# Performance work log

Measured on AMD Instinct MI355X. Metric: run time of the kernel, lower is better.

The kernel has to match this reference:

```python
import jax, jax.numpy as jnp
import numpy as np

B, N, D = 8, 1024, 256
H = 8
DH = D // H
R = 4          # relation types 0..3; adj value 4 = no relation
FF = 1024
EPS = 1e-5


def _lin(k, fan_in, shape):
    return jax.random.normal(k, shape, jnp.float32) * (1.0 / np.sqrt(fan_in))


def setup_inputs() -> dict:
    key = jax.random.key(0)
    ks = jax.random.split(key, 16)
    src = jax.random.normal(ks[0], (B, N, D), jnp.float32)
    adj_matrix = jax.random.randint(ks[1], (B, N, N), 0, 5, dtype=jnp.int32)
    Wq = _lin(ks[2], D, (D, D)); bq = jnp.zeros((D,), jnp.float32)
    Wk = _lin(ks[3], D, (D, D)); bk = jnp.zeros((D,), jnp.float32)
    Wv = _lin(ks[4], D, (R, D, D)); bv = jnp.zeros((R, D), jnp.float32)
    Wo = _lin(ks[5], D, (D, D)); bo = jnp.zeros((D,), jnp.float32)
    W1 = _lin(ks[6], D, (D, FF)); b1 = jnp.zeros((FF,), jnp.float32)
    W2 = _lin(ks[7], FF, (FF, D)); b2 = jnp.zeros((D,), jnp.float32)
    g1 = jnp.ones((D,), jnp.float32); beta1 = jnp.zeros((D,), jnp.float32)
    g2 = jnp.ones((D,), jnp.float32); beta2 = jnp.zeros((D,), jnp.float32)
    return dict(src=src, adj_matrix=adj_matrix, Wq=Wq, bq=bq, Wk=Wk, bk=bk,
                Wv=Wv, bv=bv, Wo=Wo, bo=bo, W1=W1, b1=b1, W2=W2, b2=b2,
                g1=g1, beta1=beta1, g2=g2, beta2=beta2)


def _ln(x, g, b):
    m = x.mean(-1, keepdims=True)
    v = ((x - m) ** 2).mean(-1, keepdims=True)
    return (x - m) * jax.lax.rsqrt(v + EPS) * g + b


def reference(src, adj_matrix, Wq, bq, Wk, bk, Wv, bv, Wo, bo, W1, b1, W2, b2, g1, beta1, g2, beta2):
    Bb, Nn, Dm = src.shape
    h, dh = H, Dm // H
    q = (src @ Wq + bq).reshape(Bb, Nn, h, dh).transpose(0, 2, 1, 3)  # (B,H,N,dh)
    k = (src @ Wk + bk).reshape(Bb, Nn, h, dh).transpose(0, 2, 1, 3)
    scores = jnp.einsum('bhid,bhjd->bhij', q, k) / np.sqrt(dh)
    attn = jax.nn.softmax(scores, axis=-1)                             # (B,H,N,N)
    out = jnp.zeros_like(q)
    for r in range(Wv.shape[0]):  # small fixed relation loop, matches module
        v_r = (src @ Wv[r] + bv[r]).reshape(Bb, Nn, h, dh).transpose(0, 2, 1, 3)
        mask = (adj_matrix == r)[:, None]                              # (B,1,N,N)
        out = out + jnp.einsum('bhij,bhjd->bhid', attn * mask, v_r)
    attn_out = out.transpose(0, 2, 1, 3).reshape(Bb, Nn, Dm) @ Wo + bo
    x = _ln(src + attn_out, g1, beta1)
    ff = jax.nn.gelu(x @ W1 + b1, approximate=False) @ W2 + b2
    return _ln(x + ff, g2, beta2)
```

## Files before the change

kernel.cpp:

```cpp
#include <hip/hip_runtime.h>
#include <hip/hip_bf16.h>
#include <cmath>

constexpr int CB  = 8;
constexpr int CN  = 1024;
constexpr int CD  = 256;
constexpr int CH  = 8;
constexpr int CDH = 32;
constexpr int CR  = 4;
constexpr int CFF = 1024;
constexpr float CEPS = 1e-5f;
constexpr size_t SZH = (size_t)CB * CH * CN * CDH;

#define MODE_QK    0
#define MODE_OPROJ 1
#define MODE_FFN1  2
#define MODE_FFN2  3
#define MODE_VT    4

typedef float v4f __attribute__((ext_vector_type(4)));
typedef short v8s __attribute__((ext_vector_type(8)));

static __device__ __forceinline__ short f2bf(float f) {
    unsigned u = __builtin_bit_cast(unsigned, f);
    u += 0x7fff + ((u >> 16) & 1);
    return (short)(u >> 16);
}

static __device__ __forceinline__ void async_copy16(const void* g, void* l) {
    __builtin_amdgcn_global_load_lds(
        (const __attribute__((address_space(1))) void*)g,
        (__attribute__((address_space(3))) void*)l, 16, 0, 0);
}

template<int BM, int BN, int MODE>
__device__ __forceinline__ void gemm_body(
    const short* __restrict__ A, const short* __restrict__ Bw,
    const float* __restrict__ biasv, const float* __restrict__ add,
    void* __restrict__ dest, int M, int K, int Nw, int bx, int by, short* smem)
{
    constexpr int WTM = BM / 2, WTN = BN / 2;
    constexpr int TM = WTM / 16, TN = WTN / 16;
    short* As = smem;
    short* Bs = smem + 2 * BM * 32;

    const int t    = threadIdx.x;
    const int lane = t & 63;
    const int w    = t >> 6;
    const int quad = lane >> 4, l15 = lane & 15;
    const int wm = w >> 1, wn = w & 1;
    const int m0 = bx * BM, n0 = by * BN;

    const int srow = lane >> 2;
    const int scol = (lane & 3) * 8;

    v4f acc[TM][TN];
    #pragma unroll
    for (int i = 0; i < TM; ++i)
        #pragma unroll
        for (int j = 0; j < TN; ++j) acc[i][j] = (v4f){0.f, 0.f, 0.f, 0.f};

    const int NK = K >> 5;

    auto stage = [&](int buf, int kt) {
        #pragma unroll
        for (int u = 0; u < BM / 64; ++u) {
            const int e0 = (w * (BM / 64) + u) * 512;
            const int row = (e0 >> 5) + srow;
            async_copy16(A + (size_t)(m0 + row) * K + kt + scol,
                         &As[buf * BM * 32 + e0]);
        }
        #pragma unroll
        for (int u = 0; u < BN / 64; ++u) {
            const int e0 = (w * (BN / 64) + u) * 512;
            const int row = (e0 >> 5) + srow;
            async_copy16(Bw + (size_t)(n0 + row) * K + kt + scol,
                         &Bs[buf * BN * 32 + e0]);
        }
    };

    stage(0, 0);

    for (int it = 0; it < NK; ++it) {
        __syncthreads();
        if (it + 1 < NK) stage((it + 1) & 1, (it + 1) << 5);

        const int buf = it & 1;
        v8s af[TM], bfr[TN];
        #pragma unroll
        for (int i = 0; i < TM; ++i)
            af[i] = *(const v8s*)&As[buf * BM * 32 +
                                     (wm * WTM + i * 16 + l15) * 32 + quad * 8];
        #pragma unroll
        for (int j = 0; j < TN; ++j)
            bfr[j] = *(const v8s*)&Bs[buf * BN * 32 +
                                      (wn * WTN + j * 16 + l15) * 32 + quad * 8];
        #pragma unroll
        for (int i = 0; i < TM; ++i)
            #pragma unroll
            for (int j = 0; j < TN; ++j)
                acc[i][j] = __builtin_amdgcn_mfma_f32_16x16x32_bf16(
                    af[i], bfr[j], acc[i][j], 0, 0, 0);
    }

    #pragma unroll
    for (int i = 0; i < TM; ++i) {
        #pragma unroll
        for (int j = 0; j < TN; ++j) {
            const int mb = m0 + wm * WTM + i * 16 + quad * 4;
            const int n  = n0 + wn * WTN + j * 16 + l15;
            float vals[4];
            if (MODE == MODE_VT) {
                #pragma unroll
                for (int rr = 0; rr < 4; ++rr) vals[rr] = acc[i][j][rr] + biasv[mb + rr];
            } else {
                #pragma unroll
                for (int rr = 0; rr < 4; ++rr) vals[rr] = acc[i][j][rr] + biasv[n];
            }

            if (MODE == MODE_QK) {
                const int b = mb >> 10, ii0 = mb & 1023;
                const int plane = n >> 8, nn = n & 255;
                const int h = nn >> 5, d = nn & 31;
                #pragma unroll
                for (int rr = 0; rr < 4; ++rr)
                    ((short*)dest)[(size_t)plane * SZH +
                        (((size_t)(b * CH + h)) * CN + ii0 + rr) * CDH + d] =
                        f2bf(vals[rr]);
            } else if (MODE == MODE_VT) {
                const int b = n >> 10, ii = n & 1023;
                #pragma unroll
                for (int rr = 0; rr < 4; ++rr) {
                    const int m = mb + rr;
                    const int r2 = m >> 8, hd = m & 255;
                    const int h = hd >> 5, d = hd & 31;
                    ((short*)dest)[2 * SZH +
                        (((size_t)(r2 * 64 + b * CH + h)) * CDH + d) * CN + ii] =
                        f2bf(vals[rr]);
                }
            } else if (MODE == MODE_OPROJ || MODE == MODE_FFN2) {
                #pragma unroll
                for (int rr = 0; rr < 4; ++rr) {
                    const size_t idx = (size_t)(mb + rr) * Nw + n;
                    ((float*)dest)[idx] = vals[rr] + add[idx];
                }
            } else {
                #pragma unroll
                for (int rr = 0; rr < 4; ++rr) {
                    const size_t idx = (size_t)(mb + rr) * Nw + n;
                    const float xx = vals[rr];
                    const float E = exp2f(2.302217f * (xx + 0.044715f * xx * xx * xx));
                    ((short*)dest)[idx] = f2bf(xx * E / (E + 1.f));
                }
            }
        }
    }
}

template<int BM, int BN, int MODE>
__global__ __launch_bounds__(256)
void gemm_mfma(const short* __restrict__ A, const short* __restrict__ Bw,
               const float* __restrict__ biasv, const float* __restrict__ add,
               void* __restrict__ dest, int M, int K, int Nw)
{
    extern __shared__ short smem[];
    gemm_body<BM, BN, MODE>(A, Bw, biasv, add, dest, M, K, Nw,
                            blockIdx.x, blockIdx.y, smem);
}

__global__ __launch_bounds__(256)
void proj_kernel(const short* __restrict__ src_bf, const short* __restrict__ wqkvT,
                 const float* __restrict__ bpack, short* __restrict__ qkv)
{
    extern __shared__ short smem[];
    const int g = blockIdx.x;
    if (g < 512) {
        gemm_body<64, 128, MODE_QK>(src_bf, wqkvT, bpack, nullptr, qkv,
                                    8192, 256, 512, g >> 2, g & 3, smem);
    } else {
        const int h2 = g - 512;
        gemm_body<64, 128, MODE_VT>(wqkvT + 512 * 256, src_bf, bpack + 512, nullptr,
                                    qkv, 1024, 256, 8192, h2 & 15, h2 >> 4, smem);
    }
}

__global__ __launch_bounds__(256)
void prep(const int* __restrict__ adj, const float* __restrict__ src,
          const float* __restrict__ Wq, const float* __restrict__ Wk,
          const float* __restrict__ Wv, const float* __restrict__ Wo,
          const float* __restrict__ W1, const float* __restrict__ W2,
          const float* __restrict__ bq, const float* __restrict__ bk,
          const float* __restrict__ bv, const float* __restrict__ bo,
          const float* __restrict__ b1, const float* __restrict__ b2,
          unsigned char* __restrict__ adj8, short* __restrict__ src_bf,
          short* __restrict__ wqkvT, short* __restrict__ woT,
          short* __restrict__ w1T, short* __restrict__ w2T,
          float* __restrict__ bpack)
{
    const int bx = blockIdx.x, t = threadIdx.x;
    if (bx < 8192) {
        const int i = bx * 256 + t;
        const int4 vv = ((const int4*)adj)[i];
        uchar4 c;
        c.x = (unsigned char)vv.x; c.y = (unsigned char)vv.y;
        c.z = (unsigned char)vv.z; c.w = (unsigned char)vv.w;
        ((uchar4*)adj8)[i] = c;
    } else if (bx < 10240) {
        const int i = (bx - 8192) * 256 + t;
        const float4 v = ((const float4*)src)[i];
        short4 o;
        o.x = f2bf(v.x); o.y = f2bf(v.y); o.z = f2bf(v.z); o.w = f2bf(v.w);
        ((short4*)src_bf)[i] = o;
    } else if (bx < 11776) {
        const int idx = (bx - 10240) * 256 + t;
        const int n = idx >> 8, k = idx & 255;
        float v;
        if (n < 256)      v = Wq[k * 256 + n];
        else if (n < 512) v = Wk[k * 256 + (n - 256)];
        else { const int r = (n - 512) >> 8;
               v = Wv[((size_t)r * 256 + k) * 256 + ((n - 512) & 255)]; }
        wqkvT[idx] = f2bf(v);
    } else if (bx < 12032) {
        const int idx = (bx - 11776) * 256 + t;
        const int n = idx >> 8, k = idx & 255;
        woT[idx] = f2bf(Wo[k * 256 + n]);
    } else if (bx < 13056) {
        const int idx = (bx - 12032) * 256 + t;
        const int n = idx >> 8, k = idx & 255;
        w1T[idx] = f2bf(W1[k * 1024 + n]);
    } else if (bx < 14080) {
        const int idx = (bx - 13056) * 256 + t;
        const int n = idx >> 10, k = idx & 1023;
        w2T[idx] = f2bf(W2[k * 256 + n]);
    } else {
        const int idx = (bx - 14080) * 256 + t;
        float bvv;
        if (idx < 256)       bvv = bq[idx];
        else if (idx < 512)  bvv = bk[idx - 256];
        else if (idx < 1536) bvv = bv[idx - 512];
        else if (idx < 1792) bvv = bo[idx - 1536];
        else if (idx < 2816) bvv = b1[idx - 1792];
        else                 bvv = b2[idx - 2816];
        bpack[idx] = bvv;
    }
}

__global__ __launch_bounds__(256)
void attn_mfma(const short* __restrict__ qg, const short* __restrict__ kg,
               const short* __restrict__ vt, const unsigned char* __restrict__ adj8,
               short* __restrict__ outh)
{
    __shared__ __align__(16) short ks[64 * 32];
    __shared__ __align__(16) short vtile[4][32][72];
    __shared__ __align__(16) short ps[64][68];
    __shared__ __align__(16) unsigned char adjs[64][72];
    __shared__ int lut[64][4];

    const int t    = threadIdx.x;
    const int lane = t & 63;
    const int w    = t >> 6;
    const int quad = lane >> 4;
    const int l15  = lane & 15;
    const int i0   = blockIdx.x * 64;
    const int h    = blockIdx.y;
    const int b    = blockIdx.z;
    const int bhh  = b * CH + h;
    const size_t bh = (size_t)bhh;

    if (t < 64) {
        const int b0 = t & 7, b1 = t >> 3;
        #pragma unroll
        for (int r = 0; r < 4; ++r) {
            const int lo = (b0 == r) ? 0x0100 : 0x0c0c;
            const int hi = (b1 == r) ? 0x0302 : 0x0c0c;
            lut[t][r] = lo | (hi << 16);
        }
    }

    const v8s qfrag = *(const v8s*)&qg[(bh * CN + i0 + 16 * w + l15) * CDH + quad * 8];

    v4f oacc[2];
    oacc[0] = (v4f){0.f, 0.f, 0.f, 0.f};
    oacc[1] = (v4f){0.f, 0.f, 0.f, 0.f};
    float plsum[4] = {0.f, 0.f, 0.f, 0.f};

    const float cs = 0.25503480f;
    const int arow = 16 * w + l15;

    const int srow = lane >> 2;
    const int scol = (lane & 3) * 8;
    const int vd0  = lane >> 3;
    const int vc   = (lane & 7) * 8;
    const short* vplane = vt + (((size_t)(w * 64 + bhh)) * CDH) * CN;
    const int aro = t >> 2;
    const int aco = (t & 3) * 16;

    for (int jt = 0; jt < 16; ++jt) {
        const int j0 = jt * 64;
        __syncthreads();

        async_copy16(kg + (bh * CN + j0 + 16 * w + srow) * CDH + scol,
                     &ks[(16 * w + srow) * 32]);
        #pragma unroll
        for (int it = 0; it < 4; ++it) {
            const int d = vd0 + 8 * it;
            const v8s vv = *(const v8s*)&vplane[(size_t)d * CN + j0 + vc];
            *(v8s*)&vtile[w][d][vc] = vv;
        }
        const int4 av = *(const int4*)&adj8[((size_t)b * CN + i0 + aro) * CN + j0 + aco];
        *(int4*)&adjs[aro][aco] = av;
        __syncthreads();

        v4f sacc[4];
        #pragma unroll
        for (int jb = 0; jb < 4; ++jb) {
            const v8s kfrag = *(const v8s*)&ks[(16 * jb + l15) * 32 + quad * 8];
            sacc[jb] = __builtin_amdgcn_mfma_f32_16x16x32_bf16(
                qfrag, kfrag, (v4f){0.f, 0.f, 0.f, 0.f}, 0, 0, 0);
        }

        #pragma unroll
        for (int rr = 0; rr < 4; ++rr) {
            const int prow = 16 * w + quad * 4 + rr;
            float p[4];
            #pragma unroll
            for (int jb = 0; jb < 4; ++jb) p[jb] = exp2f(cs * sacc[jb][rr]);
            plsum[rr] += (p[0] + p[1]) + (p[2] + p[3]);
            #pragma unroll
            for (int jb = 0; jb < 4; ++jb)
                ps[prow][16 * jb + l15] = f2bf(p[jb]);
        }

        #pragma unroll
        for (int kb = 0; kb < 2; ++kb) {
            const int2 p0 = *(const int2*)&ps[arow][32 * kb + quad * 8];
            const int2 p1 = *(const int2*)&ps[arow][32 * kb + quad * 8 + 4];
            const int2 ab = *(const int2*)&adjs[arow][32 * kb + quad * 8];
            int pf[4][4];
            #pragma unroll
            for (int half = 0; half < 2; ++half) {
                const unsigned a = (unsigned)(half ? ab.y : ab.x);
                const int P0 = half ? p1.x : p0.x;
                const int P1 = half ? p1.y : p0.y;
                const int idxA = (a & 7) | ((a >> 5) & 0x38);
                const int idxB = ((a >> 16) & 7) | ((a >> 21) & 0x38);
                const int4 selA = *(const int4*)&lut[idxA][0];
                const int4 selB = *(const int4*)&lut[idxB][0];
                pf[0][half * 2 + 0] = __builtin_amdgcn_perm(P0, P0, selA.x);
                pf[1][half * 2 + 0] = __builtin_amdgcn_perm(P0, P0, selA.y);
                pf[2][half * 2 + 0] = __builtin_amdgcn_perm(P0, P0, selA.z);
                pf[3][half * 2 + 0] = __builtin_amdgcn_perm(P0, P0, selA.w);
                pf[0][half * 2 + 1] = __builtin_amdgcn_perm(P1, P1, selB.x);
                pf[1][half * 2 + 1] = __builtin_amdgcn_perm(P1, P1, selB.y);
                pf[2][half * 2 + 1] = __builtin_amdgcn_perm(P1, P1, selB.z);
                pf[3][half * 2 + 1] = __builtin_amdgcn_perm(P1, P1, selB.w);
            }
            #pragma unroll
            for (int r = 0; r < 4; ++r) {
                const v8s pfr = __builtin_bit_cast(v8s,
                    make_int4(pf[r][0], pf[r][1], pf[r][2], pf[r][3]));
                #pragma unroll
                for (int cb = 0; cb < 2; ++cb) {
                    const v8s vfrag = *(const v8s*)&vtile[r][16 * cb + l15][32 * kb + quad * 8];
                    oacc[cb] = __builtin_amdgcn_mfma_f32_16x16x32_bf16(
                        pfr, vfrag, oacc[cb], 0, 0, 0);
                }
            }
        }
    }

    #pragma unroll
    for (int rr = 0; rr < 4; ++rr) {
        float l = plsum[rr];
        #pragma unroll
        for (int off = 1; off < 16; off <<= 1) l += __shfl_xor(l, off);
        const float inv = 1.f / l;
        const int row = i0 + 16 * w + quad * 4 + rr;
        #pragma unroll
        for (int cb = 0; cb < 2; ++cb)
            outh[((size_t)b * CN + row) * CD + h * CDH + 16 * cb + l15] =
                f2bf(oacc[cb][rr] * inv);
    }
}

__global__ __launch_bounds__(256)
void ln_kernel(const float* __restrict__ in, const float* __restrict__ g,
               const float* __restrict__ be, float* __restrict__ out,
               short* __restrict__ outb)
{
    __shared__ float red[4];
    const int row = blockIdx.x;
    const int t = threadIdx.x;
    const float x = in[(size_t)row * CD + t];

    float s = x;
    #pragma unroll
    for (int off = 32; off > 0; off >>= 1) s += __shfl_xor(s, off);
    if ((t & 63) == 0) red[t >> 6] = s;
    __syncthreads();
    const float mean = (red[0] + red[1] + red[2] + red[3]) * (1.f / CD);
    __syncthreads();

    const float dx = x - mean;
    float s2 = dx * dx;
    #pragma unroll
    for (int off = 32; off > 0; off >>= 1) s2 += __shfl_xor(s2, off);
    if ((t & 63) == 0) red[t >> 6] = s2;
    __syncthreads();
    const float var = (red[0] + red[1] + red[2] + red[3]) * (1.f / CD);

    const float y = dx * rsqrtf(var + CEPS) * g[t] + be[t];
    out[(size_t)row * CD + t] = y;
    if (outb) outb[(size_t)row * CD + t] = f2bf(y);
}

extern "C" void kernel_launch(void* const* d_in, const int* in_sizes, int n_in,
                              void* d_out, int out_size, void* d_ws, size_t ws_size,
                              hipStream_t stream)
{
    const float* src = (const float*)d_in[0];
    const int*   adj = (const int*)d_in[1];
    const float* Wq  = (const float*)d_in[2];
    const float* bq  = (const float*)d_in[3];
    const float* Wk  = (const float*)d_in[4];
    const float* bk  = (const float*)d_in[5];
    const float* Wv  = (const float*)d_in[6];
    const float* bv  = (const float*)d_in[7];
    const float* Wo  = (const float*)d_in[8];
    const float* bo  = (const float*)d_in[9];
    const float* W1  = (const float*)d_in[10];
    const float* b1  = (const float*)d_in[11];
    const float* W2  = (const float*)d_in[12];
    const float* b2  = (const float*)d_in[13];
    const float* g1  = (const float*)d_in[14];
    const float* be1 = (const float*)d_in[15];
    const float* g2  = (const float*)d_in[16];
    const float* be2 = (const float*)d_in[17];
    float* out = (float*)d_out;

    char* wsb = (char*)d_ws;
    const size_t MB = (size_t)1 << 20;

    unsigned char* adj8 = (unsigned char*)(wsb);
    short* qkv_bf = (short*)(wsb + 8 * MB);
    short* src_bf = (short*)(wsb + 32 * MB);
    short* wqkvT  = (short*)(wsb + 36 * MB);
    short* woT    = (short*)(wsb + 36 * MB + 768 * 1024);
    short* w1T    = (short*)(wsb + 36 * MB + 896 * 1024);
    short* w2T    = (short*)(wsb + 36 * MB + 1408 * 1024);
    float* bpack  = (float*)(wsb + 36 * MB + 1920 * 1024);
    short* heads_bf = (short*)(wsb + 38 * MB);
    float* tmp1   = (float*)(wsb + 42 * MB);
    float* xres   = (float*)(wsb + 8 * MB);
    short* x_bf   = (short*)(wsb + 32 * MB);
    short* h1_bf  = (short*)(wsb + 16 * MB);
    float* tmp2   = tmp1;

    const int M = CB * CN;
    dim3 blk(256);

    prep<<<dim3(14092), blk, 0, stream>>>(adj, src, Wq, Wk, Wv, Wo, W1, W2,
        bq, bk, bv, bo, b1, b2, adj8, src_bf, wqkvT, woT, w1T, w2T, bpack);

    proj_kernel<<<dim3(1536), blk, 24576, stream>>>(src_bf, wqkvT, bpack, qkv_bf);

    attn_mfma<<<dim3(CN / 64, CH, CB), blk, 0, stream>>>(
        qkv_bf, qkv_bf + SZH, qkv_bf + 2 * SZH, adj8, heads_bf);

    gemm_mfma<64, 64, MODE_OPROJ><<<dim3(M / 64, CD / 64), blk, 16384, stream>>>(
        heads_bf, woT, bpack + 1536, src, tmp1, M, CD, CD);
    ln_kernel<<<dim3(M), blk, 0, stream>>>(tmp1, g1, be1, xres, x_bf);

    gemm_mfma<64, 128, MODE_FFN1><<<dim3(M / 64, CFF / 128), blk, 24576, stream>>>(
        x_bf, w1T, bpack + 1792, nullptr, h1_bf, M, CD, CFF);
    gemm_mfma<64, 64, MODE_FFN2><<<dim3(M / 64, CD / 64), blk, 16384, stream>>>(
        h1_bf, w2T, bpack + 2816, xres, tmp2, M, CFF, CD);
    ln_kernel<<<dim3(M), blk, 0, stream>>>(tmp2, g2, be2, out, nullptr);
}
```

Baseline: 246.5 us.

## Fuse output and FFN2 projections with LayerNorm; tile weight transposes in prep

Adds a gemm_ln kernel that computes a 64-row by full-256-column GEMM tile per block, then adds bias and residual and applies LayerNorm in registers. It replaces the separate O-proj/FFN2 GEMMs and the standalone ln_kernel launches, removing the fp32 temporary round-trips and two launches. The prep kernel now transposes weights through a shared-memory 64x64 tile so reads and writes are coalesced. The trade-off is fewer blocks (128 per fused GEMM), less parallelism, and larger per-thread accumulator register use.

```diff
diff --git a/kernel.cpp b/kernel.cpp
--- a/kernel.cpp
+++ b/kernel.cpp
@@ -13,9 +13,7 @@
 constexpr size_t SZH = (size_t)CB * CH * CN * CDH;
 
 #define MODE_QK    0
-#define MODE_OPROJ 1
 #define MODE_FFN1  2
-#define MODE_FFN2  3
 #define MODE_VT    4
 
 typedef float v4f __attribute__((ext_vector_type(4)));
@@ -36,8 +34,8 @@
 template<int BM, int BN, int MODE>
 __device__ __forceinline__ void gemm_body(
     const short* __restrict__ A, const short* __restrict__ Bw,
-    const float* __restrict__ biasv, const float* __restrict__ add,
-    void* __restrict__ dest, int M, int K, int Nw, int bx, int by, short* smem)
+    const float* __restrict__ biasv, void* __restrict__ dest,
+    int M, int K, int Nw, int bx, int by, short* smem)
 {
     constexpr int WTM = BM / 2, WTN = BN / 2;
     constexpr int TM = WTM / 16, TN = WTN / 16;
@@ -138,12 +136,6 @@
                         (((size_t)(r2 * 64 + b * CH + h)) * CDH + d) * CN + ii] =
                         f2bf(vals[rr]);
                 }
-            } else if (MODE == MODE_OPROJ || MODE == MODE_FFN2) {
-                #pragma unroll
-                for (int rr = 0; rr < 4; ++rr) {
-                    const size_t idx = (size_t)(mb + rr) * Nw + n;
-                    ((float*)dest)[idx] = vals[rr] + add[idx];
-                }
             } else {
                 #pragma unroll
                 for (int rr = 0; rr < 4; ++rr) {
@@ -160,11 +152,11 @@
 template<int BM, int BN, int MODE>
 __global__ __launch_bounds__(256)
 void gemm_mfma(const short* __restrict__ A, const short* __restrict__ Bw,
-               const float* __restrict__ biasv, const float* __restrict__ add,
-               void* __restrict__ dest, int M, int K, int Nw)
+               const float* __restrict__ biasv, void* __restrict__ dest,
+               int M, int K, int Nw)
 {
     extern __shared__ short smem[];
-    gemm_body<BM, BN, MODE>(A, Bw, biasv, add, dest, M, K, Nw,
+    gemm_body<BM, BN, MODE>(A, Bw, biasv, dest, M, K, Nw,
                             blockIdx.x, blockIdx.y, smem);
 }
 
@@ -175,12 +167,93 @@
     extern __shared__ short smem[];
     const int g = blockIdx.x;
     if (g < 512) {
-        gemm_body<64, 128, MODE_QK>(src_bf, wqkvT, bpack, nullptr, qkv,
+        gemm_body<64, 128, MODE_QK>(src_bf, wqkvT, bpack, qkv,
                                     8192, 256, 512, g >> 2, g & 3, smem);
     } else {
         const int h2 = g - 512;
-        gemm_body<64, 128, MODE_VT>(wqkvT + 512 * 256, src_bf, bpack + 512, nullptr,
+        gemm_body<64, 128, MODE_VT>(wqkvT + 512 * 256, src_bf, bpack + 512,
                                     qkv, 1024, 256, 8192, h2 & 15, h2 >> 4, smem);
+    }
+}
+
+template<bool WRITE_BF>
+__global__ __launch_bounds__(256)
+void gemm_ln(const short* __restrict__ A, const short* __restrict__ Bw,
+             const float* __restrict__ biasv, const float* __restrict__ add,
+             const float* __restrict__ gw, const float* __restrict__ be,
+             float* __restrict__ outf, short* __restrict__ outb, int K)
+{
+    __shared__ short As[2][64 * 32];
+    __shared__ short Bs[2][256 * 32];
+
+    const int t    = threadIdx.x;
+    const int lane = t & 63;
+    const int w    = t >> 6;
+    const int quad = lane >> 4, l15 = lane & 15;
+    const int m0   = blockIdx.x * 64;
+
+    const int srow = lane >> 2;
+    const int scol = (lane & 3) * 8;
+
+    v4f acc[16];
+    #pragma unroll
+    for (int j = 0; j < 16; ++j) acc[j] = (v4f){0.f, 0.f, 0.f, 0.f};
+
+    const int NK = K >> 5;
+
+    auto stage = [&](int buf, int kt) {
+        async_copy16(A + (size_t)(m0 + 16 * w + srow) * K + kt + scol,
+                     &As[buf][w * 512]);
+        #pragma unroll
+        for (int u = 0; u < 4; ++u) {
+            const int e0 = (w * 4 + u) * 512;
+            async_copy16(Bw + (size_t)((e0 >> 5) + srow) * K + kt + scol,
+                         &Bs[buf][e0]);
+        }
+    };
+
+    stage(0, 0);
+
+    for (int it = 0; it < NK; ++it) {
+        __syncthreads();
+        if (it + 1 < NK) stage((it + 1) & 1, (it + 1) << 5);
+
+        const int buf = it & 1;
+        const v8s af = *(const v8s*)&As[buf][(16 * w + l15) * 32 + quad * 8];
+        #pragma unroll
+        for (int j = 0; j < 16; ++j) {
+            const v8s bfr = *(const v8s*)&Bs[buf][(16 * j + l15) * 32 + quad * 8];
+            acc[j] = __builtin_amdgcn_mfma_f32_16x16x32_bf16(af, bfr, acc[j], 0, 0, 0);
+        }
+    }
+
+    #pragma unroll
+    for (int rr = 0; rr < 4; ++rr) {
+        const int row = m0 + 16 * w + quad * 4 + rr;
+        float v[16];
+        float s = 0.f;
+        #pragma unroll
+        for (int j = 0; j < 16; ++j) {
+            const int n = 16 * j + l15;
+            v[j] = acc[j][rr] + biasv[n] + add[(size_t)row * CD + n];
+            s += v[j];
+        }
+        #pragma unroll
+        for (int off = 1; off < 16; off <<= 1) s += __shfl_xor(s, off);
+        const float mean = s * (1.f / CD);
+        float s2 = 0.f;
+        #pragma unroll
+        for (int j = 0; j < 16; ++j) { v[j] -= mean; s2 += v[j] * v[j]; }
+        #pragma unroll
+        for (int off = 1; off < 16; off <<= 1) s2 += __shfl_xor(s2, off);
+        const float rstd = rsqrtf(s2 * (1.f / CD) + CEPS);
+        #pragma unroll
+        for (int j = 0; j < 16; ++j) {
+            const int n = 16 * j + l15;
+            const float y = v[j] * rstd * gw[n] + be[n];
+            outf[(size_t)row * CD + n] = y;
+            if (WRITE_BF) outb[(size_t)row * CD + n] = f2bf(y);
+        }
     }
 }
 
@@ -197,6 +270,7 @@
           short* __restrict__ w1T, short* __restrict__ w2T,
           float* __restrict__ bpack)
 {
+    __shared__ float tile[64][65];
     const int bx = blockIdx.x, t = threadIdx.x;
     if (bx < 8192) {
         const int i = bx * 256 + t;
@@ -211,29 +285,52 @@
         short4 o;
         o.x = f2bf(v.x); o.y = f2bf(v.y); o.z = f2bf(v.z); o.w = f2bf(v.w);
         ((short4*)src_bf)[i] = o;
-    } else if (bx < 11776) {
-        const int idx = (bx - 10240) * 256 + t;
-        const int n = idx >> 8, k = idx & 255;
-        float v;
-        if (n < 256)      v = Wq[k * 256 + n];
-        else if (n < 512) v = Wk[k * 256 + (n - 256)];
-        else { const int r = (n - 512) >> 8;
-               v = Wv[((size_t)r * 256 + k) * 256 + ((n - 512) & 255)]; }
-        wqkvT[idx] = f2bf(v);
-    } else if (bx < 12032) {
-        const int idx = (bx - 11776) * 256 + t;
-        const int n = idx >> 8, k = idx & 255;
-        woT[idx] = f2bf(Wo[k * 256 + n]);
-    } else if (bx < 13056) {
-        const int idx = (bx - 12032) * 256 + t;
-        const int n = idx >> 8, k = idx & 255;
-        w1T[idx] = f2bf(W1[k * 1024 + n]);
-    } else if (bx < 14080) {
-        const int idx = (bx - 13056) * 256 + t;
-        const int n = idx >> 10, k = idx & 1023;
-        w2T[idx] = f2bf(W2[k * 256 + n]);
+    } else if (bx < 10480) {
+        const int tt = bx - 10240;
+        const float* S; short* D;
+        int Sstride, Dstride, k0, srccol, dstrow;
+        if (tt < 96) {
+            const int tk = tt & 3, tn = tt >> 2;
+            const int ng = tn * 64;
+            Sstride = 256; Dstride = 256; k0 = tk * 64;
+            dstrow = tn * 64; D = wqkvT;
+            if (ng < 256)      { S = Wq; srccol = ng; }
+            else if (ng < 512) { S = Wk; srccol = ng - 256; }
+            else { const int r = (ng - 512) >> 8;
+                   S = Wv + (size_t)r * 65536; srccol = (ng - 512) & 255; }
+        } else if (tt < 112) {
+            const int u = tt - 96, tk = u & 3, tn = u >> 2;
+            S = Wo; Sstride = 256; D = woT; Dstride = 256;
+            k0 = tk * 64; srccol = tn * 64; dstrow = tn * 64;
+        } else if (tt < 176) {
+            const int u = tt - 112, tk = u & 3, tn = u >> 2;
+            S = W1; Sstride = 1024; D = w1T; Dstride = 256;
+            k0 = tk * 64; srccol = tn * 64; dstrow = tn * 64;
+        } else {
+            const int u = tt - 176, tk = u & 15, tn = u >> 4;
+            S = W2; Sstride = 256; D = w2T; Dstride = 1024;
+            k0 = tk * 64; srccol = tn * 64; dstrow = tn * 64;
+        }
+        #pragma unroll
+        for (int u2 = 0; u2 < 4; ++u2) {
+            const int kl = (t >> 4) + u2 * 16;
+            const int nl = (t & 15) * 4;
+            const float4 v = *(const float4*)&S[(size_t)(k0 + kl) * Sstride + srccol + nl];
+            tile[kl][nl + 0] = v.x; tile[kl][nl + 1] = v.y;
+            tile[kl][nl + 2] = v.z; tile[kl][nl + 3] = v.w;
+        }
+        __syncthreads();
+        #pragma unroll
+        for (int u2 = 0; u2 < 4; ++u2) {
+            const int nl = (t >> 4) + u2 * 16;
+            const int kl = (t & 15) * 4;
+            short4 o;
+            o.x = f2bf(tile[kl + 0][nl]); o.y = f2bf(tile[kl + 1][nl]);
+            o.z = f2bf(tile[kl + 2][nl]); o.w = f2bf(tile[kl + 3][nl]);
+            *(short4*)&D[(size_t)(dstrow + nl) * Dstride + k0 + kl] = o;
+        }
     } else {
-        const int idx = (bx - 14080) * 256 + t;
+        const int idx = (bx - 10480) * 256 + t;
         float bvv;
         if (idx < 256)       bvv = bq[idx];
         else if (idx < 512)  bvv = bk[idx - 256];
@@ -383,37 +480,6 @@
     }
 }
 
-__global__ __launch_bounds__(256)
-void ln_kernel(const float* __restrict__ in, const float* __restrict__ g,
-               const float* __restrict__ be, float* __restrict__ out,
-               short* __restrict__ outb)
-{
-    __shared__ float red[4];
-    const int row = blockIdx.x;
-    const int t = threadIdx.x;
-    const float x = in[(size_t)row * CD + t];
-
-    float s = x;
-    #pragma unroll
-    for (int off = 32; off > 0; off >>= 1) s += __shfl_xor(s, off);
-    if ((t & 63) == 0) red[t >> 6] = s;
-    __syncthreads();
-    const float mean = (red[0] + red[1] + red[2] + red[3]) * (1.f / CD);
-    __syncthreads();
-
-    const float dx = x - mean;
-    float s2 = dx * dx;
-    #pragma unroll
-    for (int off = 32; off > 0; off >>= 1) s2 += __shfl_xor(s2, off);
-    if ((t & 63) == 0) red[t >> 6] = s2;
-    __syncthreads();
-    const float var = (red[0] + red[1] + red[2] + red[3]) * (1.f / CD);
-
-    const float y = dx * rsqrtf(var + CEPS) * g[t] + be[t];
-    out[(size_t)row * CD + t] = y;
-    if (outb) outb[(size_t)row * CD + t] = f2bf(y);
-}
-
 extern "C" void kernel_launch(void* const* d_in, const int* in_sizes, int n_in,
                               void* d_out, int out_size, void* d_ws, size_t ws_size,
                               hipStream_t stream)
@@ -450,16 +516,14 @@
     short* w2T    = (short*)(wsb + 36 * MB + 1408 * 1024);
     float* bpack  = (float*)(wsb + 36 * MB + 1920 * 1024);
     short* heads_bf = (short*)(wsb + 38 * MB);
-    float* tmp1   = (float*)(wsb + 42 * MB);
-    float* xres   = (float*)(wsb + 8 * MB);
+    float* xres   = (float*)(wsb + 42 * MB);
     short* x_bf   = (short*)(wsb + 32 * MB);
     short* h1_bf  = (short*)(wsb + 16 * MB);
-    float* tmp2   = tmp1;
 
     const int M = CB * CN;
     dim3 blk(256);
 
-    prep<<<dim3(14092), blk, 0, stream>>>(adj, src, Wq, Wk, Wv, Wo, W1, W2,
+    prep<<<dim3(10492), blk, 0, stream>>>(adj, src, Wq, Wk, Wv, Wo, W1, W2,
         bq, bk, bv, bo, b1, b2, adj8, src_bf, wqkvT, woT, w1T, w2T, bpack);
 
     proj_kernel<<<dim3(1536), blk, 24576, stream>>>(src_bf, wqkvT, bpack, qkv_bf);
@@ -467,13 +531,12 @@
     attn_mfma<<<dim3(CN / 64, CH, CB), blk, 0, stream>>>(
         qkv_bf, qkv_bf + SZH, qkv_bf + 2 * SZH, adj8, heads_bf);
 
-    gemm_mfma<64, 64, MODE_OPROJ><<<dim3(M / 64, CD / 64), blk, 16384, stream>>>(
-        heads_bf, woT, bpack + 1536, src, tmp1, M, CD, CD);
-    ln_kernel<<<dim3(M), blk, 0, stream>>>(tmp1, g1, be1, xres, x_bf);
+    gemm_ln<true><<<dim3(M / 64), blk, 0, stream>>>(
+        heads_bf, woT, bpack + 1536, src, g1, be1, xres, x_bf, CD);
 
     gemm_mfma<64, 128, MODE_FFN1><<<dim3(M / 64, CFF / 128), blk, 24576, stream>>>(
-        x_bf, w1T, bpack + 1792, nullptr, h1_bf, M, CD, CFF);
-    gemm_mfma<64, 64, MODE_FFN2><<<dim3(M / 64, CD / 64), blk, 16384, stream>>>(
-        h1_bf, w2T, bpack + 2816, xres, tmp2, M, CFF, CD);
-    ln_kernel<<<dim3(M), blk, 0, stream>>>(tmp2, g2, be2, out, nullptr);
-}
+        x_bf, w1T, bpack + 1792, h1_bf, M, CD, CFF);
+
+    gemm_ln<false><<<dim3(M / 64), blk, 0, stream>>>(
+        h1_bf, w2T, bpack + 2816, xres, g2, be2, out, nullptr, CFF);
+}
```

Result: slower. 255.2 us (+3.5%).
